# Kernel tuning notes

Measured on AMD Instinct MI355X. Metric: run time of the kernel, lower is better.

## Reference

```python
import jax, jax.numpy as jnp
import numpy as np

N_NODES = 50000
N_EDGES = 800000
IN_FEAT = 128
HIDDEN = 128
N_CLASSES = 32


def setup_inputs() -> dict:
    key = jax.random.key(0)
    ks = jax.random.split(key, 8)
    x = jax.random.normal(ks[0], (N_NODES, IN_FEAT), dtype=jnp.float32)
    edge_index = jax.random.randint(ks[1], (2, N_EDGES), 0, N_NODES, dtype=jnp.int64)
    def glorot(k, fan_in, fan_out):
        s = jnp.sqrt(2.0 / (fan_in + fan_out)).astype(jnp.float32)
        return jax.random.normal(k, (fan_in, fan_out), dtype=jnp.float32) * s
    W1 = glorot(ks[2], IN_FEAT, 2 * HIDDEN)
    b1 = jnp.zeros((2 * HIDDEN,), dtype=jnp.float32)
    W2 = glorot(ks[3], 2 * HIDDEN, HIDDEN)
    b2 = jnp.zeros((HIDDEN,), dtype=jnp.float32)
    W3 = glorot(ks[4], HIDDEN, N_CLASSES)
    b3 = jnp.zeros((N_CLASSES,), dtype=jnp.float32)
    return {"x": x, "edge_index": edge_index, "W1": W1, "b1": b1,
            "W2": W2, "b2": b2, "W3": W3, "b3": b3}


def _gcn_norm(edge_index, num_nodes):
    # PyG GCNConv default: add self-loops, symmetric normalization D^-1/2 (A+I) D^-1/2
    loops = jnp.arange(num_nodes, dtype=edge_index.dtype)
    src = jnp.concatenate([edge_index[0], loops])
    dst = jnp.concatenate([edge_index[1], loops])
    ones = jnp.ones_like(dst, dtype=jnp.float32)
    deg = jax.ops.segment_sum(ones, dst, num_segments=num_nodes)
    dinv = jnp.where(deg > 0, 1.0 / jnp.sqrt(deg), 0.0)
    norm = dinv[src] * dinv[dst]  # [E + N]
    return src, dst, norm


def _gcn_conv(x, src, dst, norm, W, b, num_nodes):
    h = x @ W                               # [N, out]
    msg = h[src] * norm[:, None]            # gather + per-edge scale, [E+N, out]
    agg = jax.ops.segment_sum(msg, dst, num_segments=num_nodes)  # scatter-add
    return agg + b


def reference(x, edge_index, W1, b1, W2, b2, W3, b3):
    n = x.shape[0]
    src, dst, norm = _gcn_norm(edge_index, n)
    h = jax.nn.relu(_gcn_conv(x, src, dst, norm, W1, b1, n))
    h = jax.nn.relu(_gcn_conv(h, src, dst, norm, W2, b2, n))
    return _gcn_conv(h, src, dst, norm, W3, b3, n)
```

## Files before the change

kernel.cpp:

```cpp
#include <hip/hip_runtime.h>
#include <hip/hip_fp16.h>

#define NN 50000
#define NE 800000
#define NBKT 391
#define P1B 256

typedef __attribute__((ext_vector_type(8))) _Float16 half8v;
typedef __attribute__((ext_vector_type(4))) float f32x4;

static inline size_t align_up(size_t x, size_t a) { return (x + a - 1) & ~(a - 1); }

union U8 {
    ushort4 u;
    __half2 h[2];
};

__device__ __forceinline__ float4 u8_to_f4(ushort4 uu) {
    U8 c;
    c.u = uu;
    float2 f01 = __half22float2(c.h[0]);
    float2 f23 = __half22float2(c.h[1]);
    return make_float4(f01.x, f01.y, f23.x, f23.y);
}

__device__ __forceinline__ ushort4 f4_to_u8(float4 v) {
    U8 c;
    c.h[0] = __floats2half2_rn(v.x, v.y);
    c.h[1] = __floats2half2_rn(v.z, v.w);
    return c.u;
}

__device__ __forceinline__ void gload_lds16(const unsigned short* g, unsigned short* l) {
    __builtin_amdgcn_global_load_lds(
        (const __attribute__((address_space(1))) unsigned int*)g,
        (__attribute__((address_space(3))) unsigned int*)l,
        16, 0, 0);
}

__device__ __forceinline__ int detect64(const int* __restrict__ e) {
    int ok = 1;
    for (int k = 1; k < 64; k += 2) ok &= (e[k] == 0);
    return ok;
}

__global__ __launch_bounds__(256) void bucket_hist(const int* __restrict__ e,
                                                   int* __restrict__ base,
                                                   const float* __restrict__ W1,
                                                   const float* __restrict__ W2,
                                                   const float* __restrict__ W3,
                                                   unsigned short* __restrict__ w1t,
                                                   unsigned short* __restrict__ w2t,
                                                   unsigned short* __restrict__ w3t,
                                                   int E) {
    __shared__ int hist[NBKT];
    const int is64 = detect64(e);
    for (int t = threadIdx.x; t < NBKT; t += 256) hist[t] = 0;
    __syncthreads();
    const int chunk = (E + P1B - 1) / P1B;
    const int b0 = blockIdx.x * chunk;
    const int b1 = min(E, b0 + chunk);
    for (int i = b0 + threadIdx.x; i < b1; i += 256) {
        int d = is64 ? e[2 * (E + i)] : e[E + i];
        atomicAdd(&hist[d >> 7], 1);
    }
    for (int i = blockIdx.x * 256 + threadIdx.x; i < 69632; i += P1B * 256) {
        const float* W;
        unsigned short* th;
        int K, M, j;
        if (i < 32768)      { W = W1; th = w1t; K = 128; M = 256; j = i; }
        else if (i < 65536) { W = W2; th = w2t; K = 256; M = 128; j = i - 32768; }
        else                { W = W3; th = w3t; K = 128; M = 32;  j = i - 65536; }
        int k = j / M, m = j % M;
        th[(size_t)m * K + k] = __half_as_ushort(__float2half_rn(W[j]));
    }
    __syncthreads();
    for (int t = threadIdx.x; t < NBKT; t += 256)
        base[blockIdx.x * NBKT + t] = hist[t];
}

__global__ __launch_bounds__(512) void colsum_scan(int* __restrict__ base,
                                                   int* __restrict__ bstart) {
    __shared__ int s[512];
    const int t = threadIdx.x;
    int total = 0;
    if (t < NBKT) {
        for (int b0 = 0; b0 < P1B; b0 += 8) {
            int v[8];
#pragma unroll
            for (int u = 0; u < 8; ++u) v[u] = base[(size_t)(b0 + u) * NBKT + t];
#pragma unroll
            for (int u = 0; u < 8; ++u) {
                int nv = v[u];
                base[(size_t)(b0 + u) * NBKT + t] = total;
                total += nv;
            }
        }
    }
    s[t] = (t < NBKT) ? total : 0;
    __syncthreads();
    for (int off = 1; off < 512; off <<= 1) {
        int tv = (t >= off) ? s[t - off] : 0;
        __syncthreads();
        s[t] += tv;
        __syncthreads();
    }
    if (t < NBKT) bstart[t] = s[t] - total;
    if (t == 0) bstart[NBKT] = s[511];
}

__global__ __launch_bounds__(256) void bucket_scatter(const int* __restrict__ e,
                                                      const int* __restrict__ bstart,
                                                      const int* __restrict__ base,
                                                      unsigned* __restrict__ pairs, int E) {
    __shared__ int cur[NBKT];
    const int is64 = detect64(e);
    for (int t = threadIdx.x; t < NBKT; t += 256)
        cur[t] = bstart[t] + base[blockIdx.x * NBKT + t];
    __syncthreads();
    const int chunk = (E + P1B - 1) / P1B;
    const int b0 = blockIdx.x * chunk;
    const int b1 = min(E, b0 + chunk);
    for (int i = b0 + threadIdx.x; i < b1; i += 256) {
        int s = is64 ? e[2 * i] : e[i];
        int d = is64 ? e[2 * (E + i)] : e[E + i];
        int pos = atomicAdd(&cur[d >> 7], 1);
        pairs[pos] = (unsigned)s | ((unsigned)(d & 127) << 16);
    }
}

__global__ __launch_bounds__(256) void bucket_finalize(const unsigned* __restrict__ pairs,
                                                       const int* __restrict__ bstart,
                                                       const float* __restrict__ x,
                                                       int* __restrict__ row_start,
                                                       int* __restrict__ deg_cnt,
                                                       float* __restrict__ dinv,
                                                       unsigned short* __restrict__ csr,
                                                       unsigned short* __restrict__ xh, int n) {
    __shared__ int ldeg[128];
    __shared__ int lscan[128];
    __shared__ int cur[128];
    __shared__ float sdinv[128];
    const int bkt = blockIdx.x;
    const int s0 = bstart[bkt], s1 = bstart[bkt + 1];
    if (threadIdx.x < 128) ldeg[threadIdx.x] = 0;
    __syncthreads();
    for (int i = s0 + threadIdx.x; i < s1; i += 256)
        atomicAdd(&ldeg[pairs[i] >> 16], 1);
    __syncthreads();
    if (threadIdx.x < 128) lscan[threadIdx.x] = ldeg[threadIdx.x];
    __syncthreads();
    for (int off = 1; off < 128; off <<= 1) {
        int v = 0;
        if (threadIdx.x < 128 && threadIdx.x >= off) v = lscan[threadIdx.x - off];
        __syncthreads();
        if (threadIdx.x < 128) lscan[threadIdx.x] += v;
        __syncthreads();
    }
    if (threadIdx.x < 128) {
        int node = (bkt << 7) + threadIdx.x;
        int exc = s0 + lscan[threadIdx.x] - ldeg[threadIdx.x];
        cur[threadIdx.x] = exc;
        float di = rsqrtf((float)(ldeg[threadIdx.x] + 1));
        sdinv[threadIdx.x] = di;
        if (node < n) {
            row_start[node] = exc;
            deg_cnt[node] = ldeg[threadIdx.x];
            dinv[node] = di;
        }
    }
    __syncthreads();
    for (int i = s0 + threadIdx.x; i < s1; i += 256) {
        unsigned pr = pairs[i];
        int pos = atomicAdd(&cur[pr >> 16], 1);
        csr[pos] = (unsigned short)(pr & 0xFFFFu);
    }
    for (int idx = threadIdx.x; idx < 128 * 32; idx += 256) {
        int ln = idx >> 5;
        int c4 = idx & 31;
        int node = (bkt << 7) + ln;
        if (node < n) {
            float4 v = ((const float4*)x)[(size_t)node * 32 + c4];
            float s = sdinv[ln];
            v.x *= s; v.y *= s; v.z *= s; v.w *= s;
            ((ushort4*)xh)[(size_t)node * 32 + c4] = f4_to_u8(v);
        }
    }
}

template <int BM, int BN, int WM, int WN, bool BIAS, bool RELU, bool OUTF16, bool SCALE>
__global__ __launch_bounds__(256) void gemm_f16(
    const unsigned short* __restrict__ A,
    const unsigned short* __restrict__ Wt,
    const float* __restrict__ bias, const float* __restrict__ dscale,
    float* __restrict__ Cf, unsigned short* __restrict__ Ch,
    int N, int K, int M) {
    constexpr int KS = 64;
    constexpr int WTM = BM / WM;
    constexpr int WTN = BN / WN;
    constexpr int FM = WTM / 16;
    constexpr int FN = WTN / 16;
    constexpr int ACH = BM * 8;
    constexpr int WCH = BN * 8;
    __shared__ unsigned short sA[BM][KS], sW[BN][KS];

    const int tid = threadIdx.x;
    const int lane = tid & 63;
    const int w = tid >> 6;
    const int wr = w / WN, wc = w % WN;
    const int row0 = blockIdx.y * BM;
    const int col0 = blockIdx.x * BN;

    f32x4 acc[FM][FN];
#pragma unroll
    for (int m = 0; m < FM; ++m)
#pragma unroll
        for (int nn = 0; nn < FN; ++nn) {
            f32x4 z = {0.f, 0.f, 0.f, 0.f};
            acc[m][nn] = z;
        }

    for (int k0 = 0; k0 < K; k0 += KS) {
#pragma unroll
        for (int b = 0; b < ACH; b += 256) {
            int idx = b + tid;
            int r = idx >> 3, s = idx & 7;
            int gr = row0 + r;
            int sp = s ^ (r & 7);
            if (gr < N)
                gload_lds16(&A[(size_t)gr * K + k0 + sp * 8], &sA[0][0] + idx * 8);
        }
#pragma unroll
        for (int b = 0; b < WCH; b += 256) {
            int idx = b + tid;
            int r = idx >> 3, s = idx & 7;
            int gc = col0 + r;
            int sp = s ^ (r & 7);
            gload_lds16(&Wt[(size_t)gc * K + k0 + sp * 8], &sW[0][0] + idx * 8);
        }
        __syncthreads();

        half8v af[FM][2], wf[FN][2];
        const int rsel = lane & 15;
        const int cb = lane >> 4;
#pragma unroll
        for (int m = 0; m < FM; ++m) {
            int rr = wr * WTM + m * 16 + rsel;
            af[m][0] = *(const half8v*)&sA[rr][((cb) ^ (rr & 7)) * 8];
            af[m][1] = *(const half8v*)&sA[rr][((cb + 4) ^ (rr & 7)) * 8];
        }
#pragma unroll
        for (int nn = 0; nn < FN; ++nn) {
            int rr = wc * WTN + nn * 16 + rsel;
            wf[nn][0] = *(const half8v*)&sW[rr][((cb) ^ (rr & 7)) * 8];
            wf[nn][1] = *(const half8v*)&sW[rr][((cb + 4) ^ (rr & 7)) * 8];
        }
#pragma unroll
        for (int m = 0; m < FM; ++m)
#pragma unroll
            for (int nn = 0; nn < FN; ++nn) {
                acc[m][nn] = __builtin_amdgcn_mfma_f32_16x16x32_f16(af[m][0], wf[nn][0], acc[m][nn], 0, 0, 0);
                acc[m][nn] = __builtin_amdgcn_mfma_f32_16x16x32_f16(af[m][1], wf[nn][1], acc[m][nn], 0, 0, 0);
            }
        __syncthreads();
    }

#pragma unroll
    for (int m = 0; m < FM; ++m) {
#pragma unroll
        for (int r = 0; r < 4; ++r) {
            int row = row0 + wr * WTM + m * 16 + (lane >> 4) * 4 + r;
            if (row >= N) continue;
            float rs = SCALE ? dscale[row] : 1.f;
#pragma unroll
            for (int nn = 0; nn < FN; ++nn) {
                int col = col0 + wc * WTN + nn * 16 + (lane & 15);
                float v = acc[m][nn][r];
                if (BIAS) v += bias[col];
                if (RELU) v = fmaxf(v, 0.f);
                if (SCALE) v *= rs;
                if constexpr (OUTF16) {
                    Ch[(size_t)row * M + col] = __half_as_ushort(__float2half_rn(v));
                } else {
                    Cf[(size_t)row * M + col] = v;
                }
            }
        }
    }
}

__device__ __forceinline__ float4 add4(float4 v, float4 a) {
    a.x += v.x; a.y += v.y; a.z += v.z; a.w += v.w;
    return a;
}

template <int F, int NPB, bool BIAS, bool RELU, bool OUTF16>
__global__ __launch_bounds__((F / 4) * NPB) void agg4h(
    const unsigned short* __restrict__ h, const int* __restrict__ row_start,
    const int* __restrict__ deg_cnt, const unsigned short* __restrict__ csr,
    const float* __restrict__ dinv, const float* __restrict__ bias,
    float* __restrict__ outf, unsigned short* __restrict__ outh, int n) {
    constexpr int L = F / 4;
    const int local = threadIdx.x / L;
    const int lane = threadIdx.x % L;
    const int node = blockIdx.x * NPB + local;
    if (node >= n) return;

    const ushort4* __restrict__ h4 = (const ushort4*)h;
    const float di = dinv[node];

    float4 acc0 = u8_to_f4(h4[(size_t)node * L + lane]);
    float4 acc1 = make_float4(0.f, 0.f, 0.f, 0.f);

    const int beg = row_start[node];
    const int num = deg_cnt[node];
    for (int e = 0; e < num; e += 16) {
        int c[16];
        ushort4 raw[16];
#pragma unroll
        for (int u = 0; u < 16; ++u) {
            int idx = min(e + u, num - 1);
            c[u] = csr[beg + idx];
        }
#pragma unroll
        for (int u = 0; u < 16; ++u) raw[u] = h4[(size_t)c[u] * L + lane];
#pragma unroll
        for (int u = 0; u < 8; ++u) {
            float4 v = u8_to_f4(raw[u]);
            if (e + u < num) acc0 = add4(v, acc0);
        }
#pragma unroll
        for (int u = 8; u < 16; ++u) {
            float4 v = u8_to_f4(raw[u]);
            if (e + u < num) acc1 = add4(v, acc1);
        }
    }
    float4 acc = add4(acc1, acc0);
    acc.x *= di; acc.y *= di; acc.z *= di; acc.w *= di;
    if (BIAS) {
        const float4 b = ((const float4*)bias)[lane];
        acc.x += b.x; acc.y += b.y; acc.z += b.z; acc.w += b.w;
    }
    if (RELU) {
        acc.x = fmaxf(acc.x, 0.f); acc.y = fmaxf(acc.y, 0.f);
        acc.z = fmaxf(acc.z, 0.f); acc.w = fmaxf(acc.w, 0.f);
    }
    if constexpr (OUTF16) {
        ((ushort4*)outh)[(size_t)node * L + lane] = f4_to_u8(acc);
    } else {
        ((float4*)outf)[(size_t)node * L + lane] = acc;
    }
}

extern "C" void kernel_launch(void* const* d_in, const int* in_sizes, int n_in,
                              void* d_out, int out_size, void* d_ws, size_t ws_size,
                              hipStream_t stream) {
    const float* x   = (const float*)d_in[0];
    const int*   eix = (const int*)d_in[1];
    const float* W1  = (const float*)d_in[2];
    const float* b1  = (const float*)d_in[3];
    const float* W2  = (const float*)d_in[4];
    const float* b2  = (const float*)d_in[5];
    const float* W3  = (const float*)d_in[6];
    const float* b3  = (const float*)d_in[7];
    float* out = (float*)d_out;

    const int n = NN, E = NE;

    char* p = (char*)d_ws;
    auto alloc = [&](size_t bytes) { void* r = (void*)p; p += align_up(bytes, 256); return r; };
    int*   deg_cnt   = (int*)alloc((size_t)n * 4);
    float* dinv      = (float*)alloc((size_t)n * 4);
    int*   row_start = (int*)alloc((size_t)n * 4);
    int*   bstart    = (int*)alloc((size_t)(NBKT + 1) * 4);
    int*   base      = (int*)alloc((size_t)P1B * NBKT * 4);
    unsigned* pairs  = (unsigned*)alloc((size_t)E * 4);
    unsigned short* csr = (unsigned short*)alloc((size_t)E * 2);
    unsigned short* w1t = (unsigned short*)alloc((size_t)128 * 256 * 2);
    unsigned short* w2t = (unsigned short*)alloc((size_t)256 * 128 * 2);
    unsigned short* w3t = (unsigned short*)alloc((size_t)128 * 32 * 2);
    unsigned short* xh   = (unsigned short*)alloc((size_t)n * 128 * 2);
    unsigned short* agg0 = (unsigned short*)alloc((size_t)n * 128 * 2);
    unsigned short* h1   = (unsigned short*)alloc((size_t)n * 256 * 2);
    unsigned short* h2s  = (unsigned short*)alloc((size_t)n * 128 * 2);
    unsigned short* x3   = (unsigned short*)alloc((size_t)n * 128 * 2);
    unsigned short* h3s  = (unsigned short*)alloc((size_t)n * 32 * 2);
    (void)ws_size; (void)in_sizes; (void)n_in; (void)out_size;

    bucket_hist<<<P1B, 256, 0, stream>>>(eix, base, W1, W2, W3, w1t, w2t, w3t, E);
    colsum_scan<<<1, 512, 0, stream>>>(base, bstart);
    bucket_scatter<<<P1B, 256, 0, stream>>>(eix, bstart, base, pairs, E);
    bucket_finalize<<<NBKT, 256, 0, stream>>>(pairs, bstart, x, row_start, deg_cnt,
                                              dinv, csr, xh, n);

    const int RB = (n + 127) / 128;

    agg4h<128, 8, false, false, true><<<(n + 7) / 8, 256, 0, stream>>>(
        xh, row_start, deg_cnt, csr, dinv, nullptr, nullptr, agg0, n);
    gemm_f16<128, 128, 2, 2, true, true, true, false><<<dim3(2, RB), 256, 0, stream>>>(
        agg0, w1t, b1, nullptr, nullptr, h1, n, 128, 256);

    gemm_f16<128, 128, 2, 2, false, false, true, true><<<dim3(1, RB), 256, 0, stream>>>(
        h1, w2t, nullptr, dinv, nullptr, h2s, n, 256, 128);
    agg4h<128, 8, true, true, true><<<(n + 7) / 8, 256, 0, stream>>>(
        h2s, row_start, deg_cnt, csr, dinv, b2, nullptr, x3, n);

    gemm_f16<128, 32, 4, 1, false, false, true, true><<<dim3(1, RB), 256, 0, stream>>>(
        x3, w3t, nullptr, dinv, nullptr, h3s, n, 128, 32);
    agg4h<32, 32, true, false, false><<<(n + 31) / 32, 256, 0, stream>>>(
        h3s, row_start, deg_cnt, csr, dinv, b3, out, nullptr, n);
}
```

Before: 173.3 us.

## Fuse layer-1 and layer-2 GEMMs through LDS and pack node row info

Replaces the two back-to-back GEMMs (agg0·W1 with bias and ReLU, then h1·W2 with dinv scaling) with one kernel. Each 128-row tile's hidden activations are kept in shared memory in two 128-column halves, so the 50000x256 f16 h1 intermediate is never written to or read from global memory. It also packs row_start and deg_cnt into one int2 so the aggregation kernels do a single load per node. The cost is a larger LDS footprint (about 98KB per block), which limits occupancy, and a grid of only 391 blocks.

```diff
diff --git a/kernel.cpp b/kernel.cpp
--- a/kernel.cpp
+++ b/kernel.cpp
@@ -132,8 +132,7 @@
 __global__ __launch_bounds__(256) void bucket_finalize(const unsigned* __restrict__ pairs,
                                                        const int* __restrict__ bstart,
                                                        const float* __restrict__ x,
-                                                       int* __restrict__ row_start,
-                                                       int* __restrict__ deg_cnt,
+                                                       int2* __restrict__ ninfo,
                                                        float* __restrict__ dinv,
                                                        unsigned short* __restrict__ csr,
                                                        unsigned short* __restrict__ xh, int n) {
@@ -164,8 +163,7 @@
         float di = rsqrtf((float)(ldeg[threadIdx.x] + 1));
         sdinv[threadIdx.x] = di;
         if (node < n) {
-            row_start[node] = exc;
-            deg_cnt[node] = ldeg[threadIdx.x];
+            ninfo[node] = make_int2(exc, ldeg[threadIdx.x]);
             dinv[node] = di;
         }
     }
@@ -186,6 +184,152 @@
             ((ushort4*)xh)[(size_t)node * 32 + c4] = f4_to_u8(v);
         }
     }
+}
+
+__global__ __launch_bounds__(256) void gemm12(
+    const unsigned short* __restrict__ A,
+    const unsigned short* __restrict__ W1t,
+    const unsigned short* __restrict__ W2t,
+    const float* __restrict__ b1,
+    const float* __restrict__ dinv,
+    unsigned short* __restrict__ H2,
+    int N) {
+    __shared__ unsigned short sA[128][128];
+    __shared__ unsigned short sW[128][128];
+    __shared__ unsigned short sH[128][136];
+
+    const int tid = threadIdx.x;
+    const int lane = tid & 63;
+    const int w = tid >> 6;
+    const int wr = w >> 1, wc = w & 1;
+    const int row0 = blockIdx.x * 128;
+    const int rsel = lane & 15;
+    const int cq = lane >> 4;
+
+#pragma unroll
+    for (int b = 0; b < 2048; b += 256) {
+        int idx = b + tid;
+        int r = idx >> 4, s = idx & 15;
+        int gr = row0 + r;
+        int sp = (s & 8) | ((s ^ r) & 7);
+        if (gr < N) gload_lds16(&A[(size_t)gr * 128 + sp * 8], &sA[0][0] + idx * 8);
+    }
+
+    f32x4 acc2[4][4];
+#pragma unroll
+    for (int m = 0; m < 4; ++m)
+#pragma unroll
+        for (int nn = 0; nn < 4; ++nn) {
+            f32x4 z = {0.f, 0.f, 0.f, 0.f};
+            acc2[m][nn] = z;
+        }
+
+    for (int half = 0; half < 2; ++half) {
+        __syncthreads();
+#pragma unroll
+        for (int b = 0; b < 2048; b += 256) {
+            int idx = b + tid;
+            int r = idx >> 4, s = idx & 15;
+            int sp = (s & 8) | ((s ^ r) & 7);
+            gload_lds16(&W1t[(size_t)(half * 128 + r) * 128 + sp * 8], &sW[0][0] + idx * 8);
+        }
+        __syncthreads();
+
+        f32x4 acc1[4][4];
+#pragma unroll
+        for (int m = 0; m < 4; ++m)
+#pragma unroll
+            for (int nn = 0; nn < 4; ++nn) {
+                f32x4 z = {0.f, 0.f, 0.f, 0.f};
+                acc1[m][nn] = z;
+            }
+#pragma unroll
+        for (int ks = 0; ks < 4; ++ks) {
+            half8v af[4], wf[4];
+            int c = ks * 4 + cq;
+#pragma unroll
+            for (int m = 0; m < 4; ++m) {
+                int rr = wr * 64 + m * 16 + rsel;
+                int cp = (c & 8) | ((c ^ rr) & 7);
+                af[m] = *(const half8v*)&sA[rr][cp * 8];
+            }
+#pragma unroll
+            for (int nn = 0; nn < 4; ++nn) {
+                int rr = wc * 64 + nn * 16 + rsel;
+                int cp = (c & 8) | ((c ^ rr) & 7);
+                wf[nn] = *(const half8v*)&sW[rr][cp * 8];
+            }
+#pragma unroll
+            for (int m = 0; m < 4; ++m)
+#pragma unroll
+                for (int nn = 0; nn < 4; ++nn)
+                    acc1[m][nn] = __builtin_amdgcn_mfma_f32_16x16x32_f16(af[m], wf[nn], acc1[m][nn], 0, 0, 0);
+        }
+
+        float b1v[4];
+#pragma unroll
+        for (int nn = 0; nn < 4; ++nn)
+            b1v[nn] = b1[half * 128 + wc * 64 + nn * 16 + rsel];
+#pragma unroll
+        for (int m = 0; m < 4; ++m)
+#pragma unroll
+            for (int nn = 0; nn < 4; ++nn)
+#pragma unroll
+                for (int r = 0; r < 4; ++r) {
+                    int rl = wr * 64 + m * 16 + cq * 4 + r;
+                    int cl = wc * 64 + nn * 16 + rsel;
+                    float v = fmaxf(acc1[m][nn][r] + b1v[nn], 0.f);
+                    sH[rl][cl] = __half_as_ushort(__float2half_rn(v));
+                }
+        __syncthreads();
+
+#pragma unroll
+        for (int b = 0; b < 2048; b += 256) {
+            int idx = b + tid;
+            int r = idx >> 4, s = idx & 15;
+            int sp = (s & 8) | ((s ^ r) & 7);
+            gload_lds16(&W2t[(size_t)r * 256 + half * 128 + sp * 8], &sW[0][0] + idx * 8);
+        }
+        __syncthreads();
+
+#pragma unroll
+        for (int ks = 0; ks < 4; ++ks) {
+            half8v ah[4], wf[4];
+            int koff = ks * 32 + cq * 8;
+            int c = ks * 4 + cq;
+#pragma unroll
+            for (int m = 0; m < 4; ++m) {
+                int rr = wr * 64 + m * 16 + rsel;
+                ah[m] = *(const half8v*)&sH[rr][koff];
+            }
+#pragma unroll
+            for (int nn = 0; nn < 4; ++nn) {
+                int rr = wc * 64 + nn * 16 + rsel;
+                int cp = (c & 8) | ((c ^ rr) & 7);
+                wf[nn] = *(const half8v*)&sW[rr][cp * 8];
+            }
+#pragma unroll
+            for (int m = 0; m < 4; ++m)
+#pragma unroll
+                for (int nn = 0; nn < 4; ++nn)
+                    acc2[m][nn] = __builtin_amdgcn_mfma_f32_16x16x32_f16(ah[m], wf[nn], acc2[m][nn], 0, 0, 0);
+        }
+    }
+
+#pragma unroll
+    for (int m = 0; m < 4; ++m)
+#pragma unroll
+        for (int r = 0; r < 4; ++r) {
+            int row = row0 + wr * 64 + m * 16 + cq * 4 + r;
+            if (row >= N) continue;
+            float rs = dinv[row];
+#pragma unroll
+            for (int nn = 0; nn < 4; ++nn) {
+                int col = wc * 64 + nn * 16 + rsel;
+                H2[(size_t)row * 128 + col] =
+                    __half_as_ushort(__float2half_rn(acc2[m][nn][r] * rs));
+            }
+        }
 }
 
 template <int BM, int BN, int WM, int WN, bool BIAS, bool RELU, bool OUTF16, bool SCALE>
@@ -296,8 +440,8 @@
 
 template <int F, int NPB, bool BIAS, bool RELU, bool OUTF16>
 __global__ __launch_bounds__((F / 4) * NPB) void agg4h(
-    const unsigned short* __restrict__ h, const int* __restrict__ row_start,
-    const int* __restrict__ deg_cnt, const unsigned short* __restrict__ csr,
+    const unsigned short* __restrict__ h, const int2* __restrict__ ninfo,
+    const unsigned short* __restrict__ csr,
     const float* __restrict__ dinv, const float* __restrict__ bias,
     float* __restrict__ outf, unsigned short* __restrict__ outh, int n) {
     constexpr int L = F / 4;
@@ -308,12 +452,13 @@
 
     const ushort4* __restrict__ h4 = (const ushort4*)h;
     const float di = dinv[node];
+    const int2 info = ninfo[node];
+    const int beg = info.x;
+    const int num = info.y;
 
     float4 acc0 = u8_to_f4(h4[(size_t)node * L + lane]);
     float4 acc1 = make_float4(0.f, 0.f, 0.f, 0.f);
 
-    const int beg = row_start[node];
-    const int num = deg_cnt[node];
     for (int e = 0; e < num; e += 16) {
         int c[16];
         ushort4 raw[16];
@@ -369,9 +514,8 @@
 
     char* p = (char*)d_ws;
     auto alloc = [&](size_t bytes) { void* r = (void*)p; p += align_up(bytes, 256); return r; };
-    int*   deg_cnt   = (int*)alloc((size_t)n * 4);
+    int2*  ninfo     = (int2*)alloc((size_t)n * 8);
     float* dinv      = (float*)alloc((size_t)n * 4);
-    int*   row_start = (int*)alloc((size_t)n * 4);
     int*   bstart    = (int*)alloc((size_t)(NBKT + 1) * 4);
     int*   base      = (int*)alloc((size_t)P1B * NBKT * 4);
     unsigned* pairs  = (unsigned*)alloc((size_t)E * 4);
@@ -381,7 +525,6 @@
     unsigned short* w3t = (unsigned short*)alloc((size_t)128 * 32 * 2);
     unsigned short* xh   = (unsigned short*)alloc((size_t)n * 128 * 2);
     unsigned short* agg0 = (unsigned short*)alloc((size_t)n * 128 * 2);
-    unsigned short* h1   = (unsigned short*)alloc((size_t)n * 256 * 2);
     unsigned short* h2s  = (unsigned short*)alloc((size_t)n * 128 * 2);
     unsigned short* x3   = (unsigned short*)alloc((size_t)n * 128 * 2);
     unsigned short* h3s  = (unsigned short*)alloc((size_t)n * 32 * 2);
@@ -390,23 +533,20 @@
     bucket_hist<<<P1B, 256, 0, stream>>>(eix, base, W1, W2, W3, w1t, w2t, w3t, E);
     colsum_scan<<<1, 512, 0, stream>>>(base, bstart);
     bucket_scatter<<<P1B, 256, 0, stream>>>(eix, bstart, base, pairs, E);
-    bucket_finalize<<<NBKT, 256, 0, stream>>>(pairs, bstart, x, row_start, deg_cnt,
-                                              dinv, csr, xh, n);
+    bucket_finalize<<<NBKT, 256, 0, stream>>>(pairs, bstart, x, ninfo, dinv, csr, xh, n);
 
     const int RB = (n + 127) / 128;
 
     agg4h<128, 8, false, false, true><<<(n + 7) / 8, 256, 0, stream>>>(
-        xh, row_start, deg_cnt, csr, dinv, nullptr, nullptr, agg0, n);
-    gemm_f16<128, 128, 2, 2, true, true, true, false><<<dim3(2, RB), 256, 0, stream>>>(
-        agg0, w1t, b1, nullptr, nullptr, h1, n, 128, 256);
-
-    gemm_f16<128, 128, 2, 2, false, false, true, true><<<dim3(1, RB), 256, 0, stream>>>(
-        h1, w2t, nullptr, dinv, nullptr, h2s, n, 256, 128);
+        xh, ninfo, csr, dinv, nullptr, nullptr, agg0, n);
+
+    gemm12<<<RB, 256, 0, stream>>>(agg0, w1t, w2t, b1, dinv, h2s, n);
+
     agg4h<128, 8, true, true, true><<<(n + 7) / 8, 256, 0, stream>>>(
-        h2s, row_start, deg_cnt, csr, dinv, b2, nullptr, x3, n);
+        h2s, ninfo, csr, dinv, b2, nullptr, x3, n);
 
     gemm_f16<128, 32, 4, 1, false, false, true, true><<<dim3(1, RB), 256, 0, stream>>>(
         x3, w3t, nullptr, dinv, nullptr, h3s, n, 128, 32);
     agg4h<32, 32, true, false, false><<<(n + 31) / 32, 256, 0, stream>>>(
-        h3s, row_start, deg_cnt, csr, dinv, b3, out, nullptr, n);
-}
+        h3s, ninfo, csr, dinv, b3, out, nullptr, n);
+}
```

Result: faster. 159.5 us (-8.0%).
